# Performance work log

Hardware: AMD Instinct MI355X
Metric: run time of the kernel (lower is better)

Reference implementation:

```python
import jax, jax.numpy as jnp
import numpy as np

NUM_HEADS = 12
DROP = 0.5


def setup_inputs() -> dict:
    key = jax.random.key(0)
    k1, k2, k3, k4 = jax.random.split(key, 4)
    B, N, C = 64, 577, 768
    x = jax.random.normal(k1, (B, N, C), dtype=jnp.float32)
    mask = jax.random.uniform(k2, (B, NUM_HEADS, N - 1), dtype=jnp.float32)
    Wqkv = jax.random.normal(k3, (C, 3 * C), dtype=jnp.float32) * 0.02
    bqkv = jnp.zeros((3 * C,), dtype=jnp.float32)
    Wproj = jax.random.normal(k4, (C, C), dtype=jnp.float32) * 0.02
    bproj = jnp.zeros((C,), dtype=jnp.float32)
    return {"x": x, "mask": mask, "Wqkv": Wqkv, "bqkv": bqkv,
            "Wproj": Wproj, "bproj": bproj}


def _drop_tokens(t, idx):
    # t: [B,H,N,D]; keep CLS token, gather sorted random indices from the rest
    rest = jnp.take_along_axis(t[:, :, 1:, :], idx[..., None], axis=2)
    return jnp.concatenate([t[:, :, :1, :], rest], axis=2)


def reference(x, mask, Wqkv, bqkv, Wproj, bproj):
    B, N, C = x.shape
    H = NUM_HEADS
    D = C // H
    scale = D ** -0.5
    target_len = N - int(N * DROP)  # kept tokens incl. CLS

    qkv = (x @ Wqkv + bqkv).reshape(B, N, 3, H, D)
    qkv = jnp.transpose(qkv, (2, 0, 3, 1, 4))  # [3,B,H,N,D]
    q, k, v = qkv[0], qkv[1], qkv[2]

    # random token drop (rand branch): topk of random mask, sort indices
    _, idx = jax.lax.top_k(mask, target_len - 1)  # [B,H,target_len-1]
    idx = jnp.sort(idx, axis=-1)
    k_p = _drop_tokens(k, idx)  # [B,H,target_len,D]
    v_p = _drop_tokens(v, idx)

    attn = jax.nn.softmax(
        jnp.einsum('bhnd,bhmd->bhnm', q, k_p) * scale, axis=-1)
    out = jnp.einsum('bhnm,bhmd->bhnd', attn, v_p)
    out = jnp.transpose(out, (0, 2, 1, 3)).reshape(B, N, C)
    return out @ Wproj + bproj
```

## Files before the change

kernel.cpp:

```cpp
#include <hip/hip_runtime.h>
#include <stdint.h>

#define B_      64
#define N_TOK   577
#define C_      768
#define H_      12
#define BH_     768
#define M_ROWS  36928
#define M_PAD   36992
#define KEEP    289
#define KP      320

typedef __attribute__((ext_vector_type(8))) short   bf16x8;
typedef __attribute__((ext_vector_type(4))) float   floatx4;
typedef __attribute__((ext_vector_type(4))) short   short4v;

static __device__ __forceinline__ unsigned short f2bf(float f) {
  union { float f; unsigned u; } a; a.f = f;
  unsigned u = a.u;
  u = u + 0x7FFFu + ((u >> 16) & 1u);
  return (unsigned short)(u >> 16);
}

static __device__ __forceinline__ void gl_lds16(const void* g, void* l) {
  __builtin_amdgcn_global_load_lds(
      (const __attribute__((address_space(1))) void*)g,
      (__attribute__((address_space(3))) void*)l, 16, 0, 0);
}

__global__ void topk_kernel(const float* __restrict__ mask, int* __restrict__ pos) {
  __shared__ float vals[576];
  __shared__ int woff[9];
  int row = blockIdx.x;
  int t = threadIdx.x;
  float v = mask[(size_t)row * 576 + t];
  vals[t] = v;
  __syncthreads();
  int rank = 0;
  for (int j = 0; j < 576; ++j) {
    float u = vals[j];
    rank += ((u > v) || (u == v && j < t)) ? 1 : 0;
  }
  bool sel = rank < (KEEP - 1);
  unsigned long long ball = __ballot(sel ? 1 : 0);
  int lane = t & 63, w = t >> 6;
  int lp = __popcll(ball & ((1ull << lane) - 1ull));
  if (lane == 0) woff[w] = __popcll(ball);
  __syncthreads();
  int base = 0;
  for (int i = 0; i < w; ++i) base += woff[i];
  pos[(size_t)row * 577 + 1 + t] = sel ? (1 + base + lp) : -1;
  if (t == 0) pos[(size_t)row * 577] = 0;
}

__global__ void convx_kernel(const float* __restrict__ x, unsigned short* __restrict__ xb) {
  size_t i = ((size_t)blockIdx.x * 256 + threadIdx.x) * 4;
  short4v o;
  if (i < (size_t)M_ROWS * C_) {
    float4 v = *(const float4*)(x + i);
    o.x = (short)f2bf(v.x); o.y = (short)f2bf(v.y);
    o.z = (short)f2bf(v.z); o.w = (short)f2bf(v.w);
  } else {
    o.x = 0; o.y = 0; o.z = 0; o.w = 0;
  }
  *(short4v*)(xb + i) = o;
}

__global__ void convwT_kernel(const float* __restrict__ W, unsigned short* __restrict__ Wt,
                              int N) {
  __shared__ unsigned short tile[64 * 72];
  int n0 = blockIdx.x * 64, k0 = blockIdx.y * 64;
  int t = threadIdx.x;
  for (int p = 0; p < 4; ++p) {
    int s = p * 256 + t;
    int k = s >> 4, nc = s & 15;
    float4 v = *(const float4*)(W + (size_t)(k0 + k) * N + n0 + nc * 4);
    short4v o;
    o.x = (short)f2bf(v.x); o.y = (short)f2bf(v.y);
    o.z = (short)f2bf(v.z); o.w = (short)f2bf(v.w);
    *(short4v*)(tile + k * 72 + nc * 4) = o;
  }
  __syncthreads();
  for (int p = 0; p < 2; ++p) {
    int s = p * 256 + t;
    int n = s >> 3, kc = s & 7;
    bf16x8 o;
    for (int j = 0; j < 8; ++j) o[j] = (short)tile[(kc * 8 + j) * 72 + n];
    *(bf16x8*)(Wt + (size_t)(n0 + n) * 768 + k0 + kc * 8) = o;
  }
}

__global__ void zeropad_kernel(unsigned short* __restrict__ Kp, unsigned short* __restrict__ Vp) {
  size_t idx = (size_t)blockIdx.x * 256 + threadIdx.x;
  int bh = (int)(idx / (31 * 64));
  int rem = (int)(idx % (31 * 64));
  int r = KEEP + rem / 64, d = rem & 63;
  size_t o = ((size_t)bh * KP + r) * 64 + d;
  Kp[o] = 0; Vp[o] = 0;
}

static __device__ __forceinline__ void stage_half(const unsigned short* src,
                                                  unsigned short* lds, int tid) {
#pragma unroll
  for (int c = 0; c < 2; ++c) {
    int s = c * 256 + tid;
    int r = s >> 3, cs = s & 7;
    int gc = (cs ^ (r & 7)) << 3;
    gl_lds16(src + (size_t)r * 768 + gc, lds + s * 8);
  }
}

static __device__ __forceinline__ void gemm8_core(
    const unsigned short* __restrict__ A, const unsigned short* __restrict__ Bt,
    int m0, int n0, int tid, unsigned short* As, unsigned short* Bs,
    floatx4 (&acc)[4][4]) {
  const int lane = tid & 63, wv = tid >> 6;
  const int quad = lane >> 4, lcol = lane & 15;
  const int wm = wv & 1, wn = wv >> 1;
  const int swz = lcol & 7;

#define STG_A(kt, half) stage_half(A  + (size_t)(m0 + 64*(half)) * 768 + (kt)*64, \
                                   As + ((kt)&1)*8192 + (half)*4096, tid)
#define STG_B(kt, half) stage_half(Bt + (size_t)(n0 + 64*(half)) * 768 + (kt)*64, \
                                   Bs + ((kt)&1)*8192 + (half)*4096, tid)

  STG_A(0, 0); STG_A(0, 1); STG_B(0, 0); STG_B(0, 1);
  STG_A(1, 0); STG_A(1, 1); STG_B(1, 0);
  asm volatile("s_waitcnt vmcnt(6)" ::: "memory");
  __builtin_amdgcn_s_barrier();

  for (int t = 0; t < 12; ++t) {
    const unsigned short* Asl = As + (t & 1) * 8192;
    const unsigned short* Bsl = Bs + (t & 1) * 8192;

    bf16x8 af[4][2], bfr[4][2];
#pragma unroll
    for (int i = 0; i < 4; ++i)
#pragma unroll
      for (int ks = 0; ks < 2; ++ks) {
        int cc = ks * 4 + quad;
        af[i][ks]  = *(const bf16x8*)(Asl + (wm * 64 + i * 16 + lcol) * 64 + ((cc ^ swz) << 3));
        bfr[i][ks] = *(const bf16x8*)(Bsl + (wn * 64 + i * 16 + lcol) * 64 + ((cc ^ swz) << 3));
      }
    if (t + 1 < 12) STG_B(t + 1, 1);
    asm volatile("s_waitcnt lgkmcnt(0)" ::: "memory");
    __builtin_amdgcn_sched_barrier(0);
    __builtin_amdgcn_s_barrier();
    __builtin_amdgcn_s_setprio(1);
#pragma unroll
    for (int j = 0; j < 4; ++j)
#pragma unroll
      for (int ks = 0; ks < 2; ++ks)
        acc[0][j] = __builtin_amdgcn_mfma_f32_16x16x32_bf16(af[0][ks], bfr[j][ks], acc[0][j], 0, 0, 0);
    __builtin_amdgcn_s_setprio(0);
    __builtin_amdgcn_s_barrier();

#pragma unroll
    for (int p = 1; p < 4; ++p) {
      if (t + 2 < 12) {
        if (p == 1)      STG_A(t + 2, 0);
        else if (p == 2) STG_A(t + 2, 1);
        else             STG_B(t + 2, 0);
      }
      __builtin_amdgcn_s_barrier();
      __builtin_amdgcn_s_setprio(1);
#pragma unroll
      for (int j = 0; j < 4; ++j)
#pragma unroll
        for (int ks = 0; ks < 2; ++ks)
          acc[p][j] = __builtin_amdgcn_mfma_f32_16x16x32_bf16(af[p][ks], bfr[j][ks], acc[p][j], 0, 0, 0);
      __builtin_amdgcn_s_setprio(0);
      if (p == 3) {
        if (t < 10)       asm volatile("s_waitcnt vmcnt(6)" ::: "memory");
        else if (t == 10) asm volatile("s_waitcnt vmcnt(0)" ::: "memory");
      }
      __builtin_amdgcn_s_barrier();
    }
  }
#undef STG_A
#undef STG_B
}

__global__ __launch_bounds__(256) void qkv_gemm_kernel(
    const unsigned short* __restrict__ A, const unsigned short* __restrict__ Bt,
    const float* __restrict__ bias, const int* __restrict__ pos,
    unsigned short* __restrict__ Q, unsigned short* __restrict__ Kp,
    unsigned short* __restrict__ Vp) {
  __shared__ unsigned short As[2 * 8192];
  __shared__ unsigned short Bs[2 * 8192];
  const int tid = threadIdx.x;
  const int lane = tid & 63, wv = tid >> 6;
  const int quad = lane >> 4, lcol = lane & 15;
  const int wm = wv & 1, wn = wv >> 1;
  int sid = blockIdx.x;
  int m_t, n_t;
  if (sid < 5184) {
    int sb = sid / 48, r = sid % 48;
    int gm = sb % 36, gn = sb / 36;
    m_t = gm * 8 + (r & 7);
    n_t = gn * 6 + (r >> 3);
  } else { m_t = 288; n_t = sid - 5184; }
  const int m0 = m_t * 128, n0 = n_t * 128;

  floatx4 acc[4][4] = {};
  gemm8_core(A, Bt, m0, n0, tid, As, Bs, acc);

  const int nbase = n0 + wn * 64;
  const int which = nbase / 768;
  const int h = (nbase - which * 768) >> 6;
  float bv[4];
#pragma unroll
  for (int nt = 0; nt < 4; ++nt) bv[nt] = bias[nbase + nt * 16 + lcol];
#pragma unroll
  for (int mt = 0; mt < 4; ++mt) {
#pragma unroll
    for (int r = 0; r < 4; ++r) {
      int m = m0 + wm * 64 + mt * 16 + quad * 4 + r;
      if (m >= M_ROWS) continue;
      int b = m / 577, t = m - b * 577;
      int bh = b * 12 + h;
      if (which == 0) {
        size_t base = ((size_t)bh * 577 + t) * 64;
#pragma unroll
        for (int nt = 0; nt < 4; ++nt)
          Q[base + nt * 16 + lcol] = f2bf(acc[mt][nt][r] + bv[nt]);
      } else {
        int p = pos[(size_t)bh * 577 + t];
        if (p >= 0) {
          size_t base = ((size_t)bh * KP + p) * 64;
          if (which == 1) {
            int sw = p & 7;
#pragma unroll
            for (int nt = 0; nt < 4; ++nt) {
              int d = nt * 16 + lcol;
              int d2 = (d & 7) | (((d >> 3) ^ sw) << 3);
              Kp[base + d2] = f2bf(acc[mt][nt][r] + bv[nt]);
            }
          } else {
#pragma unroll
            for (int nt = 0; nt < 4; ++nt)
              Vp[base + nt * 16 + lcol] = f2bf(acc[mt][nt][r] + bv[nt]);
          }
        }
      }
    }
  }
}

__global__ void transv_kernel(const unsigned short* __restrict__ Vp,
                              unsigned short* __restrict__ VpT) {
  __shared__ unsigned short tile[64 * 72];
  int bh = blockIdx.y, p0 = blockIdx.x * 64;
  int t = threadIdx.x;
  for (int pp = 0; pp < 2; ++pp) {
    int s = pp * 256 + t;
    int p = s >> 3, dc = s & 7;
    bf16x8 v = *(const bf16x8*)(Vp + ((size_t)bh * KP + p0 + p) * 64 + dc * 8);
    *(bf16x8*)(tile + p * 72 + dc * 8) = v;
  }
  __syncthreads();
  for (int pp = 0; pp < 2; ++pp) {
    int s = pp * 256 + t;
    int d = s >> 3, pc = s & 7;
    bf16x8 o;
    for (int j = 0; j < 8; ++j) o[j] = (short)tile[(pc * 8 + j) * 72 + d];
    int pc2 = pc ^ (d & 7);
    *(bf16x8*)(VpT + ((size_t)bh * 64 + d) * KP + p0 + pc2 * 8) = o;
  }
}

__global__ __launch_bounds__(256) void attn_kernel(
    const unsigned short* __restrict__ Q, const unsigned short* __restrict__ Kp,
    const unsigned short* __restrict__ VpT, unsigned short* __restrict__ attnout) {
  __shared__ unsigned short S[320 * 64];
  __shared__ unsigned short Vs[64 * 320];
  const int tid = threadIdx.x;
  const int lane = tid & 63, w = tid >> 6;
  const int quad = lane >> 4, lcol = lane & 15;
  const int g = blockIdx.x;
  const int chunk = g / 80, within = g - chunk * 80;
  const int by = chunk * 8 + (within & 7);
  const int bx = within >> 3;
  const int q0 = bx * 64 + w * 16;

  bf16x8 aq[2];
  {
    int qr = q0 + lcol;
    if (qr < N_TOK) {
      const unsigned short* qp = Q + ((size_t)by * N_TOK + qr) * 64;
      aq[0] = *(const bf16x8*)(qp + quad * 8);
      aq[1] = *(const bf16x8*)(qp + 32 + quad * 8);
    } else {
      bf16x8 z = {0, 0, 0, 0, 0, 0, 0, 0};
      aq[0] = z; aq[1] = z;
    }
  }
  __builtin_amdgcn_sched_barrier(0);

  const unsigned short* kg = Kp + (size_t)by * KP * 64;
#pragma unroll
  for (int c = 0; c < 10; ++c) {
    int s = c * 256 + tid;
    gl_lds16(kg + s * 8, S + s * 8);
  }
  __builtin_amdgcn_sched_barrier(0);
  const unsigned short* vg = VpT + (size_t)by * 64 * KP;
#pragma unroll
  for (int c = 0; c < 10; ++c) {
    int s = c * 256 + tid;
    gl_lds16(vg + s * 8, Vs + s * 8);
  }
  __builtin_amdgcn_sched_barrier(0);

  asm volatile("s_waitcnt vmcnt(10)" ::: "memory");
  __builtin_amdgcn_sched_barrier(0);
  __builtin_amdgcn_s_barrier();

  floatx4 sacc[20] = {};
  __builtin_amdgcn_s_setprio(1);
#pragma unroll
  for (int nt = 0; nt < 19; ++nt) {
    int r16 = nt * 16 + lcol;
    const unsigned short* kb = S + r16 * 64;
    int sw = r16 & 7;
    bf16x8 b0 = *(const bf16x8*)(kb + ((quad ^ sw) << 3));
    bf16x8 b1 = *(const bf16x8*)(kb + (((quad + 4) ^ sw) << 3));
    sacc[nt] = __builtin_amdgcn_mfma_f32_16x16x32_bf16(aq[0], b0, sacc[nt], 0, 0, 0);
    sacc[nt] = __builtin_amdgcn_mfma_f32_16x16x32_bf16(aq[1], b1, sacc[nt], 0, 0, 0);
  }
  __builtin_amdgcn_s_setprio(0);

  const float scale = 0.125f;
  float inva[4];
  for (int r = 0; r < 4; ++r) {
    float mx = -1e30f;
#pragma unroll
    for (int nt = 0; nt < 20; ++nt) {
      int n = nt * 16 + lcol;
      float s = sacc[nt][r] * scale;
      if (n < KEEP) mx = fmaxf(mx, s);
    }
    for (int off = 1; off < 16; off <<= 1) mx = fmaxf(mx, __shfl_xor(mx, off, 64));
    float sum = 0.f;
#pragma unroll
    for (int nt = 0; nt < 20; ++nt) {
      int n = nt * 16 + lcol;
      float e = (n < KEEP) ? __expf(sacc[nt][r] * scale - mx) : 0.f;
      sacc[nt][r] = e;
      sum += e;
    }
    for (int off = 1; off < 16; off <<= 1) sum += __shfl_xor(sum, off, 64);
    inva[r] = 1.f / sum;
  }

  asm volatile("s_waitcnt lgkmcnt(0) vmcnt(0)" ::: "memory");
  __builtin_amdgcn_sched_barrier(0);
  __builtin_amdgcn_s_barrier();

#pragma unroll
  for (int r = 0; r < 4; ++r) {
    int rowl = w * 16 + quad * 4 + r;
    int swp = rowl & 7;
#pragma unroll
    for (int nt = 0; nt < 20; ++nt) {
      int n = nt * 16 + lcol;
      int u = n >> 3;
      int u2 = (u & 0x38) | ((u & 7) ^ swp);
      S[rowl * 320 + u2 * 8 + (n & 7)] = f2bf(sacc[nt][r] * inva[r]);
    }
  }
  asm volatile("s_waitcnt lgkmcnt(0)" ::: "memory");
  __builtin_amdgcn_sched_barrier(0);

  floatx4 oacc[4] = {};
  const int prow = w * 16 + lcol;
  const int psw = prow & 7;
  const int vsw = lcol & 7;
  __builtin_amdgcn_s_setprio(1);
#pragma unroll
  for (int kc = 0; kc < 10; ++kc) {
    int u = kc * 4 + quad;
    int pu2 = (u & 0x38) | ((u & 7) ^ psw);
    bf16x8 pa = *(const bf16x8*)(S + prow * 320 + pu2 * 8);
    int vu2 = (u & 0x38) | ((u & 7) ^ vsw);
#pragma unroll
    for (int nt = 0; nt < 4; ++nt) {
      bf16x8 vb = *(const bf16x8*)(Vs + (nt * 16 + lcol) * 320 + vu2 * 8);
      oacc[nt] = __builtin_amdgcn_mfma_f32_16x16x32_bf16(pa, vb, oacc[nt], 0, 0, 0);
    }
  }
  __builtin_amdgcn_s_setprio(0);

  int b = by / H_, h = by - b * H_;
#pragma unroll
  for (int nt = 0; nt < 4; ++nt)
#pragma unroll
    for (int r = 0; r < 4; ++r) {
      int qr = bx * 64 + w * 16 + quad * 4 + r;
      if (qr < N_TOK)
        attnout[((size_t)(b * N_TOK + qr)) * C_ + h * 64 + nt * 16 + lcol] = f2bf(oacc[nt][r]);
    }
}

__global__ __launch_bounds__(256) void proj_gemm_kernel(
    const unsigned short* __restrict__ A, const unsigned short* __restrict__ Bt,
    const float* __restrict__ bias, float* __restrict__ out) {
  __shared__ unsigned short As[2 * 8192];
  __shared__ unsigned short Bs[2 * 8192];
  const int tid = threadIdx.x;
  const int lane = tid & 63, wv = tid >> 6;
  const int quad = lane >> 4, lcol = lane & 15;
  const int wm = wv & 1, wn = wv >> 1;
  int sid = blockIdx.x;
  int m_t, n_t;
  if (sid < 1728) {
    int sb = sid / 48, r = sid % 48;
    m_t = sb * 8 + (r & 7);
    n_t = r >> 3;
  } else { m_t = 288; n_t = sid - 1728; }
  const int m0 = m_t * 128, n0 = n_t * 128;

  floatx4 acc[4][4] = {};
  gemm8_core(A, Bt, m0, n0, tid, As, Bs, acc);

  const int nbase = n0 + wn * 64;
  float bv[4];
#pragma unroll
  for (int nt = 0; nt < 4; ++nt) bv[nt] = bias[nbase + nt * 16 + lcol];
#pragma unroll
  for (int mt = 0; mt < 4; ++mt)
#pragma unroll
    for (int r = 0; r < 4; ++r) {
      int m = m0 + wm * 64 + mt * 16 + quad * 4 + r;
      if (m >= M_ROWS) continue;
#pragma unroll
      for (int nt = 0; nt < 4; ++nt)
        out[(size_t)m * C_ + nbase + nt * 16 + lcol] = acc[mt][nt][r] + bv[nt];
    }
}

extern "C" void kernel_launch(void* const* d_in, const int* in_sizes, int n_in,
                              void* d_out, int out_size, void* d_ws, size_t ws_size,
                              hipStream_t stream) {
  const float* x     = (const float*)d_in[0];
  const float* mask  = (const float*)d_in[1];
  const float* Wqkv  = (const float*)d_in[2];
  const float* bqkv  = (const float*)d_in[3];
  const float* Wproj = (const float*)d_in[4];
  const float* bproj = (const float*)d_in[5];
  float* out = (float*)d_out;

  char* ws = (char*)d_ws;
  unsigned short* xb     = (unsigned short*)(ws);
  unsigned short* attno  = xb;
  unsigned short* WqkvT  = (unsigned short*)(ws + 56819712);
  unsigned short* WprojT = (unsigned short*)(ws + 60358656);
  int*            pos    = (int*)(ws + 61538304);
  unsigned short* Qb     = (unsigned short*)(ws + 63310848);
  unsigned short* Kpb    = (unsigned short*)(ws + 120032256);
  unsigned short* Vpb    = (unsigned short*)(ws + 151489536);
  unsigned short* VpTb   = (unsigned short*)(ws + 182946816);

  hipLaunchKernelGGL(topk_kernel,     dim3(768),      dim3(576), 0, stream, mask, pos);
  hipLaunchKernelGGL(convx_kernel,    dim3(27744),    dim3(256), 0, stream, x, xb);
  hipLaunchKernelGGL(convwT_kernel,   dim3(36, 12),   dim3(256), 0, stream, Wqkv, WqkvT, 2304);
  hipLaunchKernelGGL(convwT_kernel,   dim3(12, 12),   dim3(256), 0, stream, Wproj, WprojT, 768);
  hipLaunchKernelGGL(zeropad_kernel,  dim3(5952),     dim3(256), 0, stream, Kpb, Vpb);
  hipLaunchKernelGGL(qkv_gemm_kernel, dim3(5202),     dim3(256), 0, stream, xb, WqkvT, bqkv, pos, Qb, Kpb, Vpb);
  hipLaunchKernelGGL(transv_kernel,   dim3(5, 768),   dim3(256), 0, stream, Vpb, VpTb);
  hipLaunchKernelGGL(attn_kernel,     dim3(7680),     dim3(256), 0, stream, Qb, Kpb, VpTb, attno);
  hipLaunchKernelGGL(proj_gemm_kernel,dim3(1734),     dim3(256), 0, stream, attno, WprojT, bproj, out);
}
```

Baseline: 595.4 us.

## Enlarge GEMM tiles to 256x256 with 8 waves and XCD-aware block remapping

Both the QKV and projection GEMMs move from 128x128 tiles with 4 waves to 256x256 tiles with 8 waves (512 threads). Each wave now holds a 128x64 accumulator, and the LDS double buffers double in size. Block IDs are remapped so that consecutive tiles on the same XCD share rows, which should improve L2 reuse. The larger tiles cut global and LDS traffic per FLOP, at the cost of higher register and LDS pressure, lower occupancy, and more waste on the padded M tail (M_PAD 36992 is not a multiple of 256, so the last tile row reads past the padding).

```diff
diff --git a/kernel.cpp b/kernel.cpp
--- a/kernel.cpp
+++ b/kernel.cpp
@@ -99,30 +99,30 @@
   Kp[o] = 0; Vp[o] = 0;
 }
 
-static __device__ __forceinline__ void stage_half(const unsigned short* src,
-                                                  unsigned short* lds, int tid) {
+static __device__ __forceinline__ void stage_half512(const unsigned short* src,
+                                                     unsigned short* lds, int tid) {
 #pragma unroll
   for (int c = 0; c < 2; ++c) {
-    int s = c * 256 + tid;
+    int s = c * 512 + tid;
     int r = s >> 3, cs = s & 7;
     int gc = (cs ^ (r & 7)) << 3;
     gl_lds16(src + (size_t)r * 768 + gc, lds + s * 8);
   }
 }
 
-static __device__ __forceinline__ void gemm8_core(
+static __device__ __forceinline__ void gemm256_core(
     const unsigned short* __restrict__ A, const unsigned short* __restrict__ Bt,
     int m0, int n0, int tid, unsigned short* As, unsigned short* Bs,
-    floatx4 (&acc)[4][4]) {
+    floatx4 (&acc)[8][4]) {
   const int lane = tid & 63, wv = tid >> 6;
   const int quad = lane >> 4, lcol = lane & 15;
-  const int wm = wv & 1, wn = wv >> 1;
+  const int wm = wv >> 2, wn = wv & 3;
   const int swz = lcol & 7;
 
-#define STG_A(kt, half) stage_half(A  + (size_t)(m0 + 64*(half)) * 768 + (kt)*64, \
-                                   As + ((kt)&1)*8192 + (half)*4096, tid)
-#define STG_B(kt, half) stage_half(Bt + (size_t)(n0 + 64*(half)) * 768 + (kt)*64, \
-                                   Bs + ((kt)&1)*8192 + (half)*4096, tid)
+#define STG_A(kt, half) stage_half512(A  + (size_t)(m0 + 128*(half)) * 768 + (kt)*64, \
+                                      As + ((kt)&1)*16384 + (half)*8192, tid)
+#define STG_B(kt, half) stage_half512(Bt + (size_t)(n0 + 128*(half)) * 768 + (kt)*64, \
+                                      Bs + ((kt)&1)*16384 + (half)*8192, tid)
 
   STG_A(0, 0); STG_A(0, 1); STG_B(0, 0); STG_B(0, 1);
   STG_A(1, 0); STG_A(1, 1); STG_B(1, 0);
@@ -130,28 +130,33 @@
   __builtin_amdgcn_s_barrier();
 
   for (int t = 0; t < 12; ++t) {
-    const unsigned short* Asl = As + (t & 1) * 8192;
-    const unsigned short* Bsl = Bs + (t & 1) * 8192;
-
-    bf16x8 af[4][2], bfr[4][2];
-#pragma unroll
-    for (int i = 0; i < 4; ++i)
-#pragma unroll
-      for (int ks = 0; ks < 2; ++ks) {
-        int cc = ks * 4 + quad;
-        af[i][ks]  = *(const bf16x8*)(Asl + (wm * 64 + i * 16 + lcol) * 64 + ((cc ^ swz) << 3));
-        bfr[i][ks] = *(const bf16x8*)(Bsl + (wn * 64 + i * 16 + lcol) * 64 + ((cc ^ swz) << 3));
-      }
+    const unsigned short* Asl = As + (t & 1) * 16384;
+    const unsigned short* Bsl = Bs + (t & 1) * 16384;
+
+    bf16x8 af[8][2], bfr[4][2];
+#pragma unroll
+    for (int ks = 0; ks < 2; ++ks) {
+      int cc = ks * 4 + quad;
+      int co = (cc ^ swz) << 3;
+#pragma unroll
+      for (int i = 0; i < 8; ++i)
+        af[i][ks]  = *(const bf16x8*)(Asl + (wm * 128 + i * 16 + lcol) * 64 + co);
+#pragma unroll
+      for (int j = 0; j < 4; ++j)
+        bfr[j][ks] = *(const bf16x8*)(Bsl + (wn * 64 + j * 16 + lcol) * 64 + co);
+    }
     if (t + 1 < 12) STG_B(t + 1, 1);
     asm volatile("s_waitcnt lgkmcnt(0)" ::: "memory");
     __builtin_amdgcn_sched_barrier(0);
     __builtin_amdgcn_s_barrier();
     __builtin_amdgcn_s_setprio(1);
 #pragma unroll
-    for (int j = 0; j < 4; ++j)
-#pragma unroll
-      for (int ks = 0; ks < 2; ++ks)
-        acc[0][j] = __builtin_amdgcn_mfma_f32_16x16x32_bf16(af[0][ks], bfr[j][ks], acc[0][j], 0, 0, 0);
+    for (int i = 0; i < 2; ++i)
+#pragma unroll
+      for (int j = 0; j < 4; ++j)
+#pragma unroll
+        for (int ks = 0; ks < 2; ++ks)
+          acc[i][j] = __builtin_amdgcn_mfma_f32_16x16x32_bf16(af[i][ks], bfr[j][ks], acc[i][j], 0, 0, 0);
     __builtin_amdgcn_s_setprio(0);
     __builtin_amdgcn_s_barrier();
 
@@ -165,10 +170,12 @@
       __builtin_amdgcn_s_barrier();
       __builtin_amdgcn_s_setprio(1);
 #pragma unroll
-      for (int j = 0; j < 4; ++j)
-#pragma unroll
-        for (int ks = 0; ks < 2; ++ks)
-          acc[p][j] = __builtin_amdgcn_mfma_f32_16x16x32_bf16(af[p][ks], bfr[j][ks], acc[p][j], 0, 0, 0);
+      for (int i = 2 * p; i < 2 * p + 2; ++i)
+#pragma unroll
+        for (int j = 0; j < 4; ++j)
+#pragma unroll
+          for (int ks = 0; ks < 2; ++ks)
+            acc[i][j] = __builtin_amdgcn_mfma_f32_16x16x32_bf16(af[i][ks], bfr[j][ks], acc[i][j], 0, 0, 0);
       __builtin_amdgcn_s_setprio(0);
       if (p == 3) {
         if (t < 10)       asm volatile("s_waitcnt vmcnt(6)" ::: "memory");
@@ -181,29 +188,25 @@
 #undef STG_B
 }
 
-__global__ __launch_bounds__(256) void qkv_gemm_kernel(
+__global__ __launch_bounds__(512) void qkv_gemm_kernel(
     const unsigned short* __restrict__ A, const unsigned short* __restrict__ Bt,
     const float* __restrict__ bias, const int* __restrict__ pos,
     unsigned short* __restrict__ Q, unsigned short* __restrict__ Kp,
     unsigned short* __restrict__ Vp) {
-  __shared__ unsigned short As[2 * 8192];
-  __shared__ unsigned short Bs[2 * 8192];
+  __shared__ unsigned short As[2 * 16384];
+  __shared__ unsigned short Bs[2 * 16384];
   const int tid = threadIdx.x;
   const int lane = tid & 63, wv = tid >> 6;
   const int quad = lane >> 4, lcol = lane & 15;
-  const int wm = wv & 1, wn = wv >> 1;
-  int sid = blockIdx.x;
-  int m_t, n_t;
-  if (sid < 5184) {
-    int sb = sid / 48, r = sid % 48;
-    int gm = sb % 36, gn = sb / 36;
-    m_t = gm * 8 + (r & 7);
-    n_t = gn * 6 + (r >> 3);
-  } else { m_t = 288; n_t = sid - 5184; }
-  const int m0 = m_t * 128, n0 = n_t * 128;
-
-  floatx4 acc[4][4] = {};
-  gemm8_core(A, Bt, m0, n0, tid, As, Bs, acc);
+  const int wm = wv >> 2, wn = wv & 3;
+  int orig = blockIdx.x;
+  int xcd = orig & 7, loc = orig >> 3;
+  int wgid = (xcd < 1 ? xcd * 164 : 164 + (xcd - 1) * 163) + loc;
+  const int m_t = wgid / 9, n_t = wgid % 9;
+  const int m0 = m_t * 256, n0 = n_t * 256;
+
+  floatx4 acc[8][4] = {};
+  gemm256_core(A, Bt, m0, n0, tid, As, Bs, acc);
 
   const int nbase = n0 + wn * 64;
   const int which = nbase / 768;
@@ -212,10 +215,10 @@
 #pragma unroll
   for (int nt = 0; nt < 4; ++nt) bv[nt] = bias[nbase + nt * 16 + lcol];
 #pragma unroll
-  for (int mt = 0; mt < 4; ++mt) {
+  for (int i = 0; i < 8; ++i) {
 #pragma unroll
     for (int r = 0; r < 4; ++r) {
-      int m = m0 + wm * 64 + mt * 16 + quad * 4 + r;
+      int m = m0 + wm * 128 + i * 16 + quad * 4 + r;
       if (m >= M_ROWS) continue;
       int b = m / 577, t = m - b * 577;
       int bh = b * 12 + h;
@@ -223,7 +226,7 @@
         size_t base = ((size_t)bh * 577 + t) * 64;
 #pragma unroll
         for (int nt = 0; nt < 4; ++nt)
-          Q[base + nt * 16 + lcol] = f2bf(acc[mt][nt][r] + bv[nt]);
+          Q[base + nt * 16 + lcol] = f2bf(acc[i][nt][r] + bv[nt]);
       } else {
         int p = pos[(size_t)bh * 577 + t];
         if (p >= 0) {
@@ -234,12 +237,12 @@
             for (int nt = 0; nt < 4; ++nt) {
               int d = nt * 16 + lcol;
               int d2 = (d & 7) | (((d >> 3) ^ sw) << 3);
-              Kp[base + d2] = f2bf(acc[mt][nt][r] + bv[nt]);
+              Kp[base + d2] = f2bf(acc[i][nt][r] + bv[nt]);
             }
           } else {
 #pragma unroll
             for (int nt = 0; nt < 4; ++nt)
-              Vp[base + nt * 16 + lcol] = f2bf(acc[mt][nt][r] + bv[nt]);
+              Vp[base + nt * 16 + lcol] = f2bf(acc[i][nt][r] + bv[nt]);
           }
         }
       }
@@ -402,40 +405,37 @@
     }
 }
 
-__global__ __launch_bounds__(256) void proj_gemm_kernel(
+__global__ __launch_bounds__(512) void proj_gemm_kernel(
     const unsigned short* __restrict__ A, const unsigned short* __restrict__ Bt,
     const float* __restrict__ bias, float* __restrict__ out) {
-  __shared__ unsigned short As[2 * 8192];
-  __shared__ unsigned short Bs[2 * 8192];
+  __shared__ unsigned short As[2 * 16384];
+  __shared__ unsigned short Bs[2 * 16384];
   const int tid = threadIdx.x;
   const int lane = tid & 63, wv = tid >> 6;
   const int quad = lane >> 4, lcol = lane & 15;
-  const int wm = wv & 1, wn = wv >> 1;
-  int sid = blockIdx.x;
-  int m_t, n_t;
-  if (sid < 1728) {
-    int sb = sid / 48, r = sid % 48;
-    m_t = sb * 8 + (r & 7);
-    n_t = r >> 3;
-  } else { m_t = 288; n_t = sid - 1728; }
-  const int m0 = m_t * 128, n0 = n_t * 128;
-
-  floatx4 acc[4][4] = {};
-  gemm8_core(A, Bt, m0, n0, tid, As, Bs, acc);
+  const int wm = wv >> 2, wn = wv & 3;
+  int orig = blockIdx.x;
+  int xcd = orig & 7, loc = orig >> 3;
+  int wgid = (xcd < 3 ? xcd * 55 : 165 + (xcd - 3) * 54) + loc;
+  const int m_t = wgid / 3, n_t = wgid % 3;
+  const int m0 = m_t * 256, n0 = n_t * 256;
+
+  floatx4 acc[8][4] = {};
+  gemm256_core(A, Bt, m0, n0, tid, As, Bs, acc);
 
   const int nbase = n0 + wn * 64;
   float bv[4];
 #pragma unroll
   for (int nt = 0; nt < 4; ++nt) bv[nt] = bias[nbase + nt * 16 + lcol];
 #pragma unroll
-  for (int mt = 0; mt < 4; ++mt)
+  for (int i = 0; i < 8; ++i)
 #pragma unroll
     for (int r = 0; r < 4; ++r) {
-      int m = m0 + wm * 64 + mt * 16 + quad * 4 + r;
+      int m = m0 + wm * 128 + i * 16 + quad * 4 + r;
       if (m >= M_ROWS) continue;
 #pragma unroll
       for (int nt = 0; nt < 4; ++nt)
-        out[(size_t)m * C_ + nbase + nt * 16 + lcol] = acc[mt][nt][r] + bv[nt];
+        out[(size_t)m * C_ + nbase + nt * 16 + lcol] = acc[i][nt][r] + bv[nt];
     }
 }
 
@@ -466,8 +466,8 @@
   hipLaunchKernelGGL(convwT_kernel,   dim3(36, 12),   dim3(256), 0, stream, Wqkv, WqkvT, 2304);
   hipLaunchKernelGGL(convwT_kernel,   dim3(12, 12),   dim3(256), 0, stream, Wproj, WprojT, 768);
   hipLaunchKernelGGL(zeropad_kernel,  dim3(5952),     dim3(256), 0, stream, Kpb, Vpb);
-  hipLaunchKernelGGL(qkv_gemm_kernel, dim3(5202),     dim3(256), 0, stream, xb, WqkvT, bqkv, pos, Qb, Kpb, Vpb);
+  hipLaunchKernelGGL(qkv_gemm_kernel, dim3(1305),     dim3(512), 0, stream, xb, WqkvT, bqkv, pos, Qb, Kpb, Vpb);
   hipLaunchKernelGGL(transv_kernel,   dim3(5, 768),   dim3(256), 0, stream, Vpb, VpTb);
   hipLaunchKernelGGL(attn_kernel,     dim3(7680),     dim3(256), 0, stream, Qb, Kpb, VpTb, attno);
-  hipLaunchKernelGGL(proj_gemm_kernel,dim3(1734),     dim3(256), 0, stream, attno, WprojT, bproj, out);
-}
+  hipLaunchKernelGGL(proj_gemm_kernel,dim3(435),      dim3(512), 0, stream, attno, WprojT, bproj, out);
+}
```

Measured after the change: 601.1 us. About the same (+1.0%).
